# Kernel optimization log

Hardware: AMD Instinct MI355X
Metric: run time of the kernel (lower is better)

Reference implementation:

```python
import jax, jax.numpy as jnp
import numpy as np

D_MODEL = 512
NHEAD = 8
WINDOW = 128
DFF = 2048
LN_EPS = 1e-5


def _layernorm(x, g, b):
    mu = jnp.mean(x, axis=-1, keepdims=True)
    var = jnp.mean(jnp.square(x - mu), axis=-1, keepdims=True)
    return (x - mu) * jax.lax.rsqrt(var + LN_EPS) * g + b


def setup_inputs() -> dict:
    key = jax.random.key(0)
    ks = jax.random.split(key, 8)
    d, dff = D_MODEL, DFF
    s = 0.02
    return {
        "x": jax.random.normal(ks[0], (1, 4096, d), dtype=jnp.float32),
        # weights stored [in, out] (transposed vs torch nn.Linear.weight)
        "qkv_w": jax.random.normal(ks[1], (d, 3 * d), dtype=jnp.float32) * s,
        "qkv_b": jnp.zeros((3 * d,), jnp.float32),
        "out_w": jax.random.normal(ks[2], (d, d), dtype=jnp.float32) * s,
        "out_b": jnp.zeros((d,), jnp.float32),
        "ln1_g": jnp.ones((d,), jnp.float32),
        "ln1_b": jnp.zeros((d,), jnp.float32),
        "w1": jax.random.normal(ks[3], (d, dff), dtype=jnp.float32) * s,
        "b1": jnp.zeros((dff,), jnp.float32),
        "w2": jax.random.normal(ks[4], (dff, d), dtype=jnp.float32) * s,
        "b2": jnp.zeros((d,), jnp.float32),
        "ln2_g": jnp.ones((d,), jnp.float32),
        "ln2_b": jnp.zeros((d,), jnp.float32),
    }


def reference(x, qkv_w, qkv_b, out_w, out_b, ln1_g, ln1_b, w1, b1, w2, b2, ln2_g, ln2_b):
    B, S, d = x.shape
    H = NHEAD
    hd = d // H
    # qkv projection -> [B,S,3,H,hd] -> q,k,v each [B,H,S,hd]
    qkv = (x @ qkv_w + qkv_b).reshape(B, S, 3, H, hd)
    q = jnp.transpose(qkv[:, :, 0], (0, 2, 1, 3))
    k = jnp.transpose(qkv[:, :, 1], (0, 2, 1, 3))
    v = jnp.transpose(qkv[:, :, 2], (0, 2, 1, 3))
    # NOTE: faithful to source, scale is 1/sqrt(d_model), NOT 1/sqrt(head_dim)
    scores = jnp.einsum('bhqd,bhkd->bhqk', q, k) / jnp.sqrt(jnp.float32(d))
    idx = jnp.arange(S)
    band = jnp.abs(idx[:, None] - idx[None, :]) <= WINDOW  # [S,S] window mask
    scores = jnp.where(band[None, None], scores, -jnp.inf)
    attn = jax.nn.softmax(scores, axis=-1)
    o = jnp.einsum('bhqk,bhkd->bhqd', attn, v)
    o = jnp.transpose(o, (0, 2, 1, 3)).reshape(B, S, d)
    attn_out = o @ out_w + out_b
    x1 = _layernorm(x + attn_out, ln1_g, ln1_b)
    ff = jax.nn.relu(x1 @ w1 + b1) @ w2 + b2  # dropout=0 / eval mode
    return _layernorm(x1 + ff, ln2_g, ln2_b)
```

## Files before the change

kernel.cpp:

```cpp
#include <hip/hip_runtime.h>
#include <math.h>

constexpr int D      = 512;
constexpr int NH     = 8;
constexpr int HD     = 64;
constexpr int WIN    = 128;
constexpr int DFF    = 2048;
constexpr int SEQ    = 4096;
constexpr float LN_EPS = 1e-5f;

typedef float f32x4 __attribute__((ext_vector_type(4)));
typedef __bf16 bf16x8 __attribute__((ext_vector_type(8)));

__device__ __forceinline__ unsigned short f2bf(float f) {
    union { float f; unsigned u; } v; v.f = f;
    unsigned r = v.u + 0x7FFF + ((v.u >> 16) & 1);
    return (unsigned short)(r >> 16);
}
__device__ __forceinline__ float bf2f(unsigned short u) {
    union { unsigned u; float f; } v; v.u = (unsigned)u << 16; return v.f;
}

__device__ __forceinline__ void gload16(const void* g, void* l) {
    __builtin_amdgcn_global_load_lds(
        (const __attribute__((address_space(1))) unsigned int*)g,
        (__attribute__((address_space(3))) unsigned int*)l,
        16, 0, 0);
}

__global__ __launch_bounds__(256) void prep(
    const float* __restrict__ x, unsigned short* __restrict__ xb,
    const float* __restrict__ qkv_w, const float* __restrict__ out_w,
    const float* __restrict__ w1,    const float* __restrict__ w2,
    unsigned short* __restrict__ qkvw_t, unsigned short* __restrict__ outw_t,
    unsigned short* __restrict__ w1_t,   unsigned short* __restrict__ w2_t)
{
    const int b = blockIdx.x;
    if (b < 1024) {
        int i = b * 2048 + threadIdx.x * 8;
        float4 v0 = *(const float4*)(x + i);
        float4 v1 = *(const float4*)(x + i + 4);
        ushort4 u0 = make_ushort4(f2bf(v0.x), f2bf(v0.y), f2bf(v0.z), f2bf(v0.w));
        ushort4 u1 = make_ushort4(f2bf(v1.x), f2bf(v1.y), f2bf(v1.z), f2bf(v1.w));
        *(ushort4*)(xb + i) = u0;
        *(ushort4*)(xb + i + 4) = u1;
        return;
    }
    __shared__ float t[32][33];
    const int b2 = b - 1024;
    const float* W; unsigned short* Wt; int K, N, nt, kt;
    if (b2 < 768)       { W = qkv_w; Wt = qkvw_t; K = 512;  N = 1536; nt = b2 % 48;          kt = b2 / 48; }
    else if (b2 < 1024) { W = out_w; Wt = outw_t; K = 512;  N = 512;  nt = (b2 - 768) % 16;  kt = (b2 - 768) / 16; }
    else if (b2 < 2048) { W = w1;    Wt = w1_t;   K = 512;  N = 2048; nt = (b2 - 1024) % 64; kt = (b2 - 1024) / 64; }
    else                { W = w2;    Wt = w2_t;   K = 2048; N = 512;  nt = (b2 - 2048) % 16; kt = (b2 - 2048) / 16; }
    const int tx = threadIdx.x & 31, ty = threadIdx.x >> 5;
    const int n0 = nt * 32, k0 = kt * 32;
    #pragma unroll
    for (int r = 0; r < 4; ++r)
        t[ty + r * 8][tx] = W[(size_t)(k0 + ty + r * 8) * N + n0 + tx];
    __syncthreads();
    #pragma unroll
    for (int r = 0; r < 4; ++r)
        Wt[(size_t)(n0 + ty + r * 8) * K + k0 + tx] = f2bf(t[tx][ty + r * 8]);
}

__device__ __forceinline__ void gemm_core64(
    const unsigned short* __restrict__ A, const unsigned short* __restrict__ Bt,
    int K, int m0, int n0, int kbeg, int kend, char* lds, f32x4 acc[4][4])
{
    const int tid  = threadIdx.x;
    const int lane = tid & 63;
    const int wave = tid >> 6;
    const int wr = wave >> 1, wc = wave & 1;
    const int lr = lane & 15, lk = lane >> 4;
    const int aoff = ((wr * 64 + lr) << 6) + (lk << 4);
    const int boff = ((wc * 64 + lr) << 6) + (lk << 4);
    const int srow = (tid * 16) >> 6;
    const int skb  = (tid * 16) & 63;

    for (int k0 = kbeg; k0 < kend; k0 += 64) {
        #pragma unroll
        for (int r = 0; r < 2; ++r) {
            const int row = srow + r * 64;
            const char* pa = (const char*)A + ((size_t)(m0 + row) * K + k0) * 2 + skb;
            const char* pb = (const char*)Bt + ((size_t)(n0 + row) * K + k0) * 2 + skb;
            gload16(pa,      lds +         r * 4096 + tid * 16);
            gload16(pa + 64, lds +  8192 + r * 4096 + tid * 16);
            gload16(pb,      lds + 16384 + r * 4096 + tid * 16);
            gload16(pb + 64, lds + 24576 + r * 4096 + tid * 16);
        }
        __syncthreads();

        bf16x8 af[2][4], bfv[2][4];
        #pragma unroll
        for (int m = 0; m < 4; ++m) {
            af[0][m] = *(const bf16x8*)(lds +        aoff + m * 1024);
            af[1][m] = *(const bf16x8*)(lds + 8192 + aoff + m * 1024);
        }
        #pragma unroll
        for (int n = 0; n < 4; ++n) {
            bfv[0][n] = *(const bf16x8*)(lds + 16384 + boff + n * 1024);
            bfv[1][n] = *(const bf16x8*)(lds + 24576 + boff + n * 1024);
        }
        #pragma unroll
        for (int ks = 0; ks < 2; ++ks)
            #pragma unroll
            for (int m = 0; m < 4; ++m)
                #pragma unroll
                for (int n = 0; n < 4; ++n)
                    acc[m][n] = __builtin_amdgcn_mfma_f32_16x16x32_bf16(
                        af[ks][m], bfv[ks][n], acc[m][n], 0, 0, 0);
        __syncthreads();
    }
}

template <bool RELU, bool OUT_BF16>
__global__ __launch_bounds__(256) void gemm_mfma(
    const unsigned short* __restrict__ A,
    const unsigned short* __restrict__ Bt,
    const float* __restrict__ bias,
    void* __restrict__ Cv, int M, int N, int K)
{
    __shared__ __align__(16) char lds[32768];
    const int lane = threadIdx.x & 63;
    const int wave = threadIdx.x >> 6;
    const int wr = wave >> 1, wc = wave & 1;
    const int lr = lane & 15, lk = lane >> 4;
    const int m0 = blockIdx.y * 128, n0 = blockIdx.x * 128;

    f32x4 acc[4][4];
    #pragma unroll
    for (int m = 0; m < 4; ++m)
        #pragma unroll
        for (int n = 0; n < 4; ++n) acc[m][n] = f32x4{0.f, 0.f, 0.f, 0.f};

    gemm_core64(A, Bt, K, m0, n0, 0, K, lds, acc);

    const int col0 = n0 + wc * 64 + lr;
    const int row0 = m0 + wr * 64 + lk * 4;
    #pragma unroll
    for (int m = 0; m < 4; ++m)
        #pragma unroll
        for (int n = 0; n < 4; ++n) {
            int col = col0 + n * 16;
            float bv = bias[col];
            #pragma unroll
            for (int j = 0; j < 4; ++j) {
                int row = row0 + m * 16 + j;
                float v = acc[m][n][j] + bv;
                if (RELU) v = fmaxf(v, 0.0f);
                if (OUT_BF16)
                    ((unsigned short*)Cv)[(size_t)row * N + col] = f2bf(v);
                else
                    ((float*)Cv)[(size_t)row * N + col] = v;
            }
        }
}

__global__ __launch_bounds__(256) void gemm_splitk(
    const unsigned short* __restrict__ A,
    const unsigned short* __restrict__ Bt,
    const float* __restrict__ bias,
    unsigned short* __restrict__ P, int M, int N, int K, int Kc)
{
    __shared__ __align__(16) char lds[32768];
    const int lane = threadIdx.x & 63;
    const int wave = threadIdx.x >> 6;
    const int wr = wave >> 1, wc = wave & 1;
    const int lr = lane & 15, lk = lane >> 4;
    const int m0 = blockIdx.y * 128, n0 = blockIdx.x * 128;
    const int zc = blockIdx.z;

    f32x4 acc[4][4];
    #pragma unroll
    for (int m = 0; m < 4; ++m)
        #pragma unroll
        for (int n = 0; n < 4; ++n) acc[m][n] = f32x4{0.f, 0.f, 0.f, 0.f};

    gemm_core64(A, Bt, K, m0, n0, zc * Kc, zc * Kc + Kc, lds, acc);

    unsigned short* Cp = P + (size_t)zc * M * N;
    const int col0 = n0 + wc * 64 + lr;
    const int row0 = m0 + wr * 64 + lk * 4;
    #pragma unroll
    for (int m = 0; m < 4; ++m)
        #pragma unroll
        for (int n = 0; n < 4; ++n) {
            int col = col0 + n * 16;
            float bv = (zc == 0) ? bias[col] : 0.0f;
            #pragma unroll
            for (int j = 0; j < 4; ++j) {
                int row = row0 + m * 16 + j;
                Cp[(size_t)row * N + col] = f2bf(acc[m][n][j] + bv);
            }
        }
}

__global__ __launch_bounds__(256) void gemm_qkv(
    const unsigned short* __restrict__ A,
    const unsigned short* __restrict__ Bt,
    const float* __restrict__ bias,
    unsigned short* __restrict__ qb,
    unsigned short* __restrict__ kb,
    unsigned short* __restrict__ vtb)
{
    constexpr int N = 3 * D, K = D;
    __shared__ __align__(16) char lds[32768];
    const int lane = threadIdx.x & 63;
    const int wave = threadIdx.x >> 6;
    const int wr = wave >> 1, wc = wave & 1;
    const int lr = lane & 15, lk = lane >> 4;
    const int m0 = blockIdx.y * 128, n0 = blockIdx.x * 128;

    f32x4 acc[4][4];
    #pragma unroll
    for (int m = 0; m < 4; ++m)
        #pragma unroll
        for (int n = 0; n < 4; ++n) acc[m][n] = f32x4{0.f, 0.f, 0.f, 0.f};

    gemm_core64(A, Bt, K, m0, n0, 0, K, lds, acc);

    const int col0 = n0 + wc * 64 + lr;
    const int row0 = m0 + wr * 64 + lk * 4;
    const int region = n0 >> 9;
    #pragma unroll
    for (int m = 0; m < 4; ++m)
        #pragma unroll
        for (int n = 0; n < 4; ++n) {
            const int col = col0 + n * 16;
            const float bv = bias[col];
            const int rowm = row0 + m * 16;
            if (region == 2) {
                const int cc = col - 1024, hh = cc >> 6, dd = cc & 63;
                ushort4 u = make_ushort4(f2bf(acc[m][n][0] + bv),
                                         f2bf(acc[m][n][1] + bv),
                                         f2bf(acc[m][n][2] + bv),
                                         f2bf(acc[m][n][3] + bv));
                *(ushort4*)&vtb[((size_t)(hh * 64 + dd)) * SEQ + rowm] = u;
            } else {
                const int cc = col - region * 512, hh = cc >> 6, dd = cc & 63;
                unsigned short* dst = (region == 0) ? qb : kb;
                #pragma unroll
                for (int j = 0; j < 4; ++j)
                    dst[((size_t)hh * SEQ + rowm + j) * 64 + dd] =
                        f2bf(acc[m][n][j] + bv);
            }
        }
}

__global__ __launch_bounds__(256) void attn_mfma(
    const unsigned short* __restrict__ qb,
    const unsigned short* __restrict__ kb,
    const unsigned short* __restrict__ vtb,
    unsigned short* __restrict__ o)
{
    constexpr float SCALE_L2E = 0.044194173824159216f * 1.4426950408889634f;
    __shared__ __align__(16) unsigned short P_lds[4][16][72];

    const int lane = threadIdx.x & 63;
    const int w    = threadIdx.x >> 6;
    const int i0   = blockIdx.x * 64;
    const int h    = blockIdx.y;
    const int lr = lane & 15, lg = lane >> 4;

    const unsigned short* qh = qb  + (size_t)h * SEQ * 64;
    const unsigned short* kh = kb  + (size_t)h * SEQ * 64;
    const unsigned short* vh = vtb + (size_t)h * 64 * SEQ;

    bf16x8 bq[2];
    {
        const unsigned short* qrow = qh + (size_t)(i0 + w * 16 + lr) * 64 + lg * 8;
        bq[0] = *(const bf16x8*)qrow;
        bq[1] = *(const bf16x8*)(qrow + 32);
    }

    f32x4 accO[4];
    #pragma unroll
    for (int n = 0; n < 4; ++n) accO[n] = f32x4{0.f, 0.f, 0.f, 0.f};
    float lsum = 0.0f;
    const int iq = i0 + w * 16 + lr;

    for (int c = 0; c < 5; ++c) {
        const int j0 = i0 - WIN + c * 64;
        if (j0 < 0 || j0 >= SEQ) continue;

        bf16x8 ak[2][4];
        #pragma unroll
        for (int m = 0; m < 4; ++m) {
            const unsigned short* kr = kh + (size_t)(j0 + m * 16 + lr) * 64 + lg * 8;
            ak[0][m] = *(const bf16x8*)kr;
            ak[1][m] = *(const bf16x8*)(kr + 32);
        }
        bf16x8 bv[2][4];
        #pragma unroll
        for (int n = 0; n < 4; ++n) {
            const unsigned short* vr = vh + (size_t)(n * 16 + lr) * SEQ + j0 + lg * 8;
            bv[0][n] = *(const bf16x8*)vr;
            bv[1][n] = *(const bf16x8*)(vr + 32);
        }

        f32x4 accS[4];
        #pragma unroll
        for (int m = 0; m < 4; ++m) {
            accS[m] = f32x4{0.f, 0.f, 0.f, 0.f};
            #pragma unroll
            for (int s = 0; s < 2; ++s)
                accS[m] = __builtin_amdgcn_mfma_f32_16x16x32_bf16(
                    ak[s][m], bq[s], accS[m], 0, 0, 0);
        }

        #pragma unroll
        for (int m = 0; m < 4; ++m) {
            const int kbase = j0 + m * 16 + lg * 4;
            float p0, p1, p2, p3;
            {
                int d0 = kbase + 0 - iq; bool v0 = (d0 >= -WIN) && (d0 <= WIN);
                int d1 = kbase + 1 - iq; bool v1 = (d1 >= -WIN) && (d1 <= WIN);
                int d2 = kbase + 2 - iq; bool v2 = (d2 >= -WIN) && (d2 <= WIN);
                int d3 = kbase + 3 - iq; bool v3 = (d3 >= -WIN) && (d3 <= WIN);
                p0 = v0 ? exp2f(accS[m][0] * SCALE_L2E) : 0.0f;
                p1 = v1 ? exp2f(accS[m][1] * SCALE_L2E) : 0.0f;
                p2 = v2 ? exp2f(accS[m][2] * SCALE_L2E) : 0.0f;
                p3 = v3 ? exp2f(accS[m][3] * SCALE_L2E) : 0.0f;
            }
            lsum += (p0 + p1) + (p2 + p3);
            ushort4 pk = make_ushort4(f2bf(p0), f2bf(p1), f2bf(p2), f2bf(p3));
            *(ushort4*)&P_lds[w][lr][m * 16 + lg * 4] = pk;
        }

        bf16x8 pa[2];
        pa[0] = *(const bf16x8*)&P_lds[w][lr][lg * 8];
        pa[1] = *(const bf16x8*)&P_lds[w][lr][32 + lg * 8];

        #pragma unroll
        for (int n = 0; n < 4; ++n)
            #pragma unroll
            for (int s = 0; s < 2; ++s)
                accO[n] = __builtin_amdgcn_mfma_f32_16x16x32_bf16(
                    pa[s], bv[s][n], accO[n], 0, 0, 0);
    }

    lsum += __shfl_xor(lsum, 16, 64);
    lsum += __shfl_xor(lsum, 32, 64);
    float rinv[4];
    #pragma unroll
    for (int j = 0; j < 4; ++j)
        rinv[j] = 1.0f / __shfl(lsum, lg * 4 + j, 64);

    #pragma unroll
    for (int n = 0; n < 4; ++n)
        #pragma unroll
        for (int j = 0; j < 4; ++j) {
            int row = i0 + w * 16 + lg * 4 + j;
            int col = h * 64 + n * 16 + lr;
            o[(size_t)row * D + col] = f2bf(accO[n][j] * rinv[j]);
        }
}

template <int NP, bool RES_BF16, bool OUT_BF16>
__global__ __launch_bounds__(256) void add_ln(
    const void* __restrict__ res, const unsigned short* __restrict__ P,
    size_t pstride,
    const float* __restrict__ g, const float* __restrict__ beta,
    void* __restrict__ out)
{
    const int wave = threadIdx.x >> 6;
    const int lane = threadIdx.x & 63;
    const int row = blockIdx.x * 4 + wave;
    const size_t rbase = (size_t)row * D;

    float v[8];
    float sum = 0.0f, sumsq = 0.0f;
    #pragma unroll
    for (int e = 0; e < 8; ++e) {
        int c = lane + e * 64;
        float z = RES_BF16 ? bf2f(((const unsigned short*)res)[rbase + c])
                           : ((const float*)res)[rbase + c];
        #pragma unroll
        for (int p = 0; p < NP; ++p)
            z += bf2f(P[p * pstride + rbase + c]);
        v[e] = z;
        sum += z;
        sumsq += z * z;
    }
    #pragma unroll
    for (int off = 32; off; off >>= 1) {
        sum   += __shfl_xor(sum, off, 64);
        sumsq += __shfl_xor(sumsq, off, 64);
    }
    const float mu   = sum * (1.0f / D);
    const float var  = sumsq * (1.0f / D) - mu * mu;
    const float rstd = rsqrtf(var + LN_EPS);

    #pragma unroll
    for (int e = 0; e < 8; ++e) {
        int c = lane + e * 64;
        float r = (v[e] - mu) * rstd * g[c] + beta[c];
        if (OUT_BF16) ((unsigned short*)out)[rbase + c] = f2bf(r);
        else          ((float*)out)[rbase + c] = r;
    }
}

extern "C" void kernel_launch(void* const* d_in, const int* in_sizes, int n_in,
                              void* d_out, int out_size, void* d_ws, size_t ws_size,
                              hipStream_t stream)
{
    const float* x      = (const float*)d_in[0];
    const float* qkv_w  = (const float*)d_in[1];
    const float* qkv_b  = (const float*)d_in[2];
    const float* out_w  = (const float*)d_in[3];
    const float* out_b  = (const float*)d_in[4];
    const float* ln1_g  = (const float*)d_in[5];
    const float* ln1_b  = (const float*)d_in[6];
    const float* w1     = (const float*)d_in[7];
    const float* b1     = (const float*)d_in[8];
    const float* w2     = (const float*)d_in[9];
    const float* b2     = (const float*)d_in[10];
    const float* ln2_g  = (const float*)d_in[11];
    const float* ln2_b  = (const float*)d_in[12];
    float* out = (float*)d_out;

    constexpr size_t MiB = 1u << 20;
    char* base = (char*)d_ws;
    unsigned short* xb     = (unsigned short*)(base + 0);
    unsigned short* qkvw_t = (unsigned short*)(base + 4 * MiB);
    unsigned short* outw_t = (unsigned short*)(base + 5 * MiB + 512 * 1024);
    unsigned short* w1_t   = (unsigned short*)(base + 6 * MiB);
    unsigned short* w2_t   = (unsigned short*)(base + 8 * MiB);
    unsigned short* qbuf   = (unsigned short*)(base + 10 * MiB);
    unsigned short* kbuf   = (unsigned short*)(base + 14 * MiB);
    unsigned short* vtbuf  = (unsigned short*)(base + 18 * MiB);
    unsigned short* o_b    = (unsigned short*)(base + 22 * MiB);
    unsigned short* pOut   = (unsigned short*)(base + 26 * MiB);
    unsigned short* x1b    = (unsigned short*)(base + 34 * MiB);
    unsigned short* ff1b   = (unsigned short*)(base + 38 * MiB);
    unsigned short* pFF2   = (unsigned short*)(base + 54 * MiB);

    prep<<<4096, 256, 0, stream>>>(x, xb, qkv_w, out_w, w1, w2,
                                   qkvw_t, outw_t, w1_t, w2_t);

    gemm_qkv<<<dim3(3 * D / 128, SEQ / 128), 256, 0, stream>>>(
        xb, qkvw_t, qkv_b, qbuf, kbuf, vtbuf);

    attn_mfma<<<dim3(SEQ / 64, NH), 256, 0, stream>>>(qbuf, kbuf, vtbuf, o_b);

    gemm_splitk<<<dim3(D / 128, SEQ / 128, 2), 256, 0, stream>>>(
        o_b, outw_t, out_b, pOut, SEQ, D, D, D / 2);

    add_ln<2, false, true><<<SEQ / 4, 256, 0, stream>>>(
        x, pOut, (size_t)SEQ * D, ln1_g, ln1_b, x1b);

    gemm_mfma<true, true><<<dim3(DFF / 128, SEQ / 128), 256, 0, stream>>>(
        x1b, w1_t, b1, ff1b, SEQ, DFF, D);

    gemm_splitk<<<dim3(D / 128, SEQ / 128, 4), 256, 0, stream>>>(
        ff1b, w2_t, b2, pFF2, SEQ, D, DFF, DFF / 4);

    add_ln<4, true, false><<<SEQ / 4, 256, 0, stream>>>(
        x1b, pFF2, (size_t)SEQ * D, ln2_g, ln2_b, out);
}
```

Measured before the change: 106.1 us.

## Double-buffer LDS tiles in MFMA GEMM core to overlap loads with compute

Replaces the single-buffered GEMM main loop with a two-stage ping-pong scheme. The next 64-wide K slice of A and B is prefetched into a second LDS buffer via global_load_lds while MFMAs consume the current buffer, which removes one barrier per iteration. The goal is to hide global-to-LDS latency in the QKV, output-projection, FFN and split-K GEMMs. The cost is doubling LDS per block to 64 KB, which lowers the number of resident blocks per CU.

```diff
diff --git a/kernel.cpp b/kernel.cpp
--- a/kernel.cpp
+++ b/kernel.cpp
@@ -64,7 +64,23 @@
         Wt[(size_t)(n0 + ty + r * 8) * K + k0 + tx] = f2bf(t[tx][ty + r * 8]);
 }
 
-__device__ __forceinline__ void gemm_core64(
+__device__ __forceinline__ void stage64(
+    const unsigned short* __restrict__ A, const unsigned short* __restrict__ Bt,
+    int K, int m0, int n0, int k0, char* buf, int srow, int skb, int tid)
+{
+    #pragma unroll
+    for (int r = 0; r < 2; ++r) {
+        const int row = srow + r * 64;
+        const char* pa = (const char*)A  + ((size_t)(m0 + row) * K + k0) * 2 + skb;
+        const char* pb = (const char*)Bt + ((size_t)(n0 + row) * K + k0) * 2 + skb;
+        gload16(pa,      buf +         r * 4096 + tid * 16);
+        gload16(pa + 64, buf +  8192 + r * 4096 + tid * 16);
+        gload16(pb,      buf + 16384 + r * 4096 + tid * 16);
+        gload16(pb + 64, buf + 24576 + r * 4096 + tid * 16);
+    }
+}
+
+__device__ __forceinline__ void gemm_core_db(
     const unsigned short* __restrict__ A, const unsigned short* __restrict__ Bt,
     int K, int m0, int n0, int kbeg, int kend, char* lds, f32x4 acc[4][4])
 {
@@ -78,29 +94,26 @@
     const int srow = (tid * 16) >> 6;
     const int skb  = (tid * 16) & 63;
 
+    stage64(A, Bt, K, m0, n0, kbeg, lds, srow, skb, tid);
+    __syncthreads();
+
+    int cur = 0;
     for (int k0 = kbeg; k0 < kend; k0 += 64) {
-        #pragma unroll
-        for (int r = 0; r < 2; ++r) {
-            const int row = srow + r * 64;
-            const char* pa = (const char*)A + ((size_t)(m0 + row) * K + k0) * 2 + skb;
-            const char* pb = (const char*)Bt + ((size_t)(n0 + row) * K + k0) * 2 + skb;
-            gload16(pa,      lds +         r * 4096 + tid * 16);
-            gload16(pa + 64, lds +  8192 + r * 4096 + tid * 16);
-            gload16(pb,      lds + 16384 + r * 4096 + tid * 16);
-            gload16(pb + 64, lds + 24576 + r * 4096 + tid * 16);
-        }
-        __syncthreads();
+        char* bufc = lds + cur * 32768;
+        if (k0 + 64 < kend)
+            stage64(A, Bt, K, m0, n0, k0 + 64, lds + (cur ^ 1) * 32768,
+                    srow, skb, tid);
 
         bf16x8 af[2][4], bfv[2][4];
         #pragma unroll
         for (int m = 0; m < 4; ++m) {
-            af[0][m] = *(const bf16x8*)(lds +        aoff + m * 1024);
-            af[1][m] = *(const bf16x8*)(lds + 8192 + aoff + m * 1024);
+            af[0][m] = *(const bf16x8*)(bufc +        aoff + m * 1024);
+            af[1][m] = *(const bf16x8*)(bufc + 8192 + aoff + m * 1024);
         }
         #pragma unroll
         for (int n = 0; n < 4; ++n) {
-            bfv[0][n] = *(const bf16x8*)(lds + 16384 + boff + n * 1024);
-            bfv[1][n] = *(const bf16x8*)(lds + 24576 + boff + n * 1024);
+            bfv[0][n] = *(const bf16x8*)(bufc + 16384 + boff + n * 1024);
+            bfv[1][n] = *(const bf16x8*)(bufc + 24576 + boff + n * 1024);
         }
         #pragma unroll
         for (int ks = 0; ks < 2; ++ks)
@@ -110,7 +123,9 @@
                 for (int n = 0; n < 4; ++n)
                     acc[m][n] = __builtin_amdgcn_mfma_f32_16x16x32_bf16(
                         af[ks][m], bfv[ks][n], acc[m][n], 0, 0, 0);
+
         __syncthreads();
+        cur ^= 1;
     }
 }
 
@@ -121,7 +136,7 @@
     const float* __restrict__ bias,
     void* __restrict__ Cv, int M, int N, int K)
 {
-    __shared__ __align__(16) char lds[32768];
+    __shared__ __align__(16) char lds[65536];
     const int lane = threadIdx.x & 63;
     const int wave = threadIdx.x >> 6;
     const int wr = wave >> 1, wc = wave & 1;
@@ -134,7 +149,7 @@
         #pragma unroll
         for (int n = 0; n < 4; ++n) acc[m][n] = f32x4{0.f, 0.f, 0.f, 0.f};
 
-    gemm_core64(A, Bt, K, m0, n0, 0, K, lds, acc);
+    gemm_core_db(A, Bt, K, m0, n0, 0, K, lds, acc);
 
     const int col0 = n0 + wc * 64 + lr;
     const int row0 = m0 + wr * 64 + lk * 4;
@@ -163,7 +178,7 @@
     const float* __restrict__ bias,
     unsigned short* __restrict__ P, int M, int N, int K, int Kc)
 {
-    __shared__ __align__(16) char lds[32768];
+    __shared__ __align__(16) char lds[65536];
     const int lane = threadIdx.x & 63;
     const int wave = threadIdx.x >> 6;
     const int wr = wave >> 1, wc = wave & 1;
@@ -177,7 +192,7 @@
         #pragma unroll
         for (int n = 0; n < 4; ++n) acc[m][n] = f32x4{0.f, 0.f, 0.f, 0.f};
 
-    gemm_core64(A, Bt, K, m0, n0, zc * Kc, zc * Kc + Kc, lds, acc);
+    gemm_core_db(A, Bt, K, m0, n0, zc * Kc, zc * Kc + Kc, lds, acc);
 
     unsigned short* Cp = P + (size_t)zc * M * N;
     const int col0 = n0 + wc * 64 + lr;
@@ -205,7 +220,7 @@
     unsigned short* __restrict__ vtb)
 {
     constexpr int N = 3 * D, K = D;
-    __shared__ __align__(16) char lds[32768];
+    __shared__ __align__(16) char lds[65536];
     const int lane = threadIdx.x & 63;
     const int wave = threadIdx.x >> 6;
     const int wr = wave >> 1, wc = wave & 1;
@@ -218,7 +233,7 @@
         #pragma unroll
         for (int n = 0; n < 4; ++n) acc[m][n] = f32x4{0.f, 0.f, 0.f, 0.f};
 
-    gemm_core64(A, Bt, K, m0, n0, 0, K, lds, acc);
+    gemm_core_db(A, Bt, K, m0, n0, 0, K, lds, acc);
 
     const int col0 = n0 + wc * 64 + lr;
     const int row0 = m0 + wr * 64 + lk * 4;
```

Measured after the change: 99.27 us. 1.07x faster.

## Pipeline GEMM core with four-stage async LDS ring buffer

Applied to the files above, without the earlier changes.

Replaces the synchronous load-then-compute GEMM main loop with a four-slot LDS ring fed by global_load_lds. Three K-steps of 32 are kept in flight, guarded by vmcnt waits and a single barrier per iteration. The goal is to overlap global memory latency with MFMA work. In exchange, LDS per block grows from 32 KB to 80 KB, which lowers occupancy, and the tail iterations issue dummy loads into a scratch region.

```diff
diff --git a/kernel.cpp b/kernel.cpp
--- a/kernel.cpp
+++ b/kernel.cpp
@@ -64,7 +64,23 @@
         Wt[(size_t)(n0 + ty + r * 8) * K + k0 + tx] = f2bf(t[tx][ty + r * 8]);
 }
 
-__device__ __forceinline__ void gemm_core64(
+__device__ __forceinline__ void stage32(
+    const unsigned short* __restrict__ A, const unsigned short* __restrict__ Bt,
+    int K, int m0, int n0, int k0, char* buf, int tid)
+{
+    const int srow = (tid * 16) >> 6;
+    const int skb  = (tid * 16) & 63;
+    #pragma unroll
+    for (int r = 0; r < 2; ++r) {
+        const int row = srow + r * 64;
+        gload16((const char*)A  + ((size_t)(m0 + row) * K + k0) * 2 + skb,
+                buf +        r * 4096 + tid * 16);
+        gload16((const char*)Bt + ((size_t)(n0 + row) * K + k0) * 2 + skb,
+                buf + 8192 + r * 4096 + tid * 16);
+    }
+}
+
+__device__ __forceinline__ void gemm_core_pipe(
     const unsigned short* __restrict__ A, const unsigned short* __restrict__ Bt,
     int K, int m0, int n0, int kbeg, int kend, char* lds, f32x4 acc[4][4])
 {
@@ -74,44 +90,44 @@
     const int wr = wave >> 1, wc = wave & 1;
     const int lr = lane & 15, lk = lane >> 4;
     const int aoff = ((wr * 64 + lr) << 6) + (lk << 4);
-    const int boff = ((wc * 64 + lr) << 6) + (lk << 4);
-    const int srow = (tid * 16) >> 6;
-    const int skb  = (tid * 16) & 63;
-
-    for (int k0 = kbeg; k0 < kend; k0 += 64) {
-        #pragma unroll
-        for (int r = 0; r < 2; ++r) {
-            const int row = srow + r * 64;
-            const char* pa = (const char*)A + ((size_t)(m0 + row) * K + k0) * 2 + skb;
-            const char* pb = (const char*)Bt + ((size_t)(n0 + row) * K + k0) * 2 + skb;
-            gload16(pa,      lds +         r * 4096 + tid * 16);
-            gload16(pa + 64, lds +  8192 + r * 4096 + tid * 16);
-            gload16(pb,      lds + 16384 + r * 4096 + tid * 16);
-            gload16(pb + 64, lds + 24576 + r * 4096 + tid * 16);
-        }
-        __syncthreads();
-
-        bf16x8 af[2][4], bfv[2][4];
-        #pragma unroll
-        for (int m = 0; m < 4; ++m) {
-            af[0][m] = *(const bf16x8*)(lds +        aoff + m * 1024);
-            af[1][m] = *(const bf16x8*)(lds + 8192 + aoff + m * 1024);
-        }
-        #pragma unroll
-        for (int n = 0; n < 4; ++n) {
-            bfv[0][n] = *(const bf16x8*)(lds + 16384 + boff + n * 1024);
-            bfv[1][n] = *(const bf16x8*)(lds + 24576 + boff + n * 1024);
-        }
-        #pragma unroll
-        for (int ks = 0; ks < 2; ++ks)
+    const int boff = 8192 + ((wc * 64 + lr) << 6) + (lk << 4);
+    const int nt = (kend - kbeg) >> 5;
+    char* dummy = lds + 65536;
+
+    stage32(A, Bt, K, m0, n0, kbeg,      lds,         tid);
+    stage32(A, Bt, K, m0, n0, kbeg + 32, lds + 16384, tid);
+    stage32(A, Bt, K, m0, n0, kbeg + 64, lds + 32768, tid);
+
+    for (int t = 0; t < nt; ++t) {
+        asm volatile("s_waitcnt vmcnt(8)" ::: "memory");
+        __builtin_amdgcn_s_barrier();
+        __builtin_amdgcn_sched_barrier(0);
+
+        {
+            const bool real = (t + 3) < nt;
+            const int  k3   = kbeg + (real ? (t + 3) : t) * 32;
+            char* dst = real ? (lds + ((t + 3) & 3) * 16384) : dummy;
+            stage32(A, Bt, K, m0, n0, k3, dst, tid);
+        }
+
+        const char* bufc = lds + (t & 3) * 16384;
+        bf16x8 af[4], bfv[4];
+        #pragma unroll
+        for (int m = 0; m < 4; ++m)
+            af[m] = *(const bf16x8*)(bufc + aoff + m * 1024);
+        #pragma unroll
+        for (int n = 0; n < 4; ++n)
+            bfv[n] = *(const bf16x8*)(bufc + boff + n * 1024);
+
+        #pragma unroll
+        for (int m = 0; m < 4; ++m)
             #pragma unroll
-            for (int m = 0; m < 4; ++m)
-                #pragma unroll
-                for (int n = 0; n < 4; ++n)
-                    acc[m][n] = __builtin_amdgcn_mfma_f32_16x16x32_bf16(
-                        af[ks][m], bfv[ks][n], acc[m][n], 0, 0, 0);
-        __syncthreads();
-    }
+            for (int n = 0; n < 4; ++n)
+                acc[m][n] = __builtin_amdgcn_mfma_f32_16x16x32_bf16(
+                    af[m], bfv[n], acc[m][n], 0, 0, 0);
+        __builtin_amdgcn_sched_barrier(0);
+    }
+    asm volatile("s_waitcnt vmcnt(0)" ::: "memory");
 }
 
 template <bool RELU, bool OUT_BF16>
@@ -121,7 +137,7 @@
     const float* __restrict__ bias,
     void* __restrict__ Cv, int M, int N, int K)
 {
-    __shared__ __align__(16) char lds[32768];
+    __shared__ __align__(16) char lds[81920];
     const int lane = threadIdx.x & 63;
     const int wave = threadIdx.x >> 6;
     const int wr = wave >> 1, wc = wave & 1;
@@ -134,7 +150,7 @@
         #pragma unroll
         for (int n = 0; n < 4; ++n) acc[m][n] = f32x4{0.f, 0.f, 0.f, 0.f};
 
-    gemm_core64(A, Bt, K, m0, n0, 0, K, lds, acc);
+    gemm_core_pipe(A, Bt, K, m0, n0, 0, K, lds, acc);
 
     const int col0 = n0 + wc * 64 + lr;
     const int row0 = m0 + wr * 64 + lk * 4;
@@ -163,7 +179,7 @@
     const float* __restrict__ bias,
     unsigned short* __restrict__ P, int M, int N, int K, int Kc)
 {
-    __shared__ __align__(16) char lds[32768];
+    __shared__ __align__(16) char lds[81920];
     const int lane = threadIdx.x & 63;
     const int wave = threadIdx.x >> 6;
     const int wr = wave >> 1, wc = wave & 1;
@@ -177,7 +193,7 @@
         #pragma unroll
         for (int n = 0; n < 4; ++n) acc[m][n] = f32x4{0.f, 0.f, 0.f, 0.f};
 
-    gemm_core64(A, Bt, K, m0, n0, zc * Kc, zc * Kc + Kc, lds, acc);
+    gemm_core_pipe(A, Bt, K, m0, n0, zc * Kc, zc * Kc + Kc, lds, acc);
 
     unsigned short* Cp = P + (size_t)zc * M * N;
     const int col0 = n0 + wc * 64 + lr;
@@ -205,7 +221,7 @@
     unsigned short* __restrict__ vtb)
 {
     constexpr int N = 3 * D, K = D;
-    __shared__ __align__(16) char lds[32768];
+    __shared__ __align__(16) char lds[81920];
     const int lane = threadIdx.x & 63;
     const int wave = threadIdx.x >> 6;
     const int wr = wave >> 1, wc = wave & 1;
@@ -218,7 +234,7 @@
         #pragma unroll
         for (int n = 0; n < 4; ++n) acc[m][n] = f32x4{0.f, 0.f, 0.f, 0.f};
 
-    gemm_core64(A, Bt, K, m0, n0, 0, K, lds, acc);
+    gemm_core_pipe(A, Bt, K, m0, n0, 0, K, lds, acc);
 
     const int col0 = n0 + wc * 64 + lr;
     const int row0 = m0 + wr * 64 + lk * 4;
```

Measured after the change: 104.0 us. No clear change (-1.9%).
